# Performance work log

Measured on AMD Instinct MI355X. Metric: run time of the kernel, lower is better.

Reference implementation:

```python
import jax, jax.numpy as jnp
import numpy as np

D_MODEL, D_INNER, D_STATE, DT_RANK, D_CONV = 1024, 2048, 16, 64, 4
BATCH, SEQLEN = 2, 2048


def setup_inputs() -> dict:
    key = jax.random.key(0)
    ks = jax.random.split(key, 8)
    g = lambda k, shape, scale: jax.random.normal(k, shape, jnp.float32) * scale
    hidden_states = jax.random.normal(ks[0], (BATCH, SEQLEN, D_MODEL), jnp.float32)
    W_in = g(ks[1], (2 * D_INNER, D_MODEL), D_MODEL ** -0.5)
    conv_w = g(ks[2], (D_INNER, D_CONV), D_CONV ** -0.5)
    conv_b = jnp.zeros((D_INNER,), jnp.float32)
    W_x = g(ks[3], (DT_RANK + 2 * D_STATE, D_INNER), D_INNER ** -0.5)
    dt_init_std = DT_RANK ** -0.5  # dt_scale = 1.0
    W_dt = jax.random.uniform(ks[4], (D_INNER, DT_RANK), jnp.float32, -dt_init_std, dt_init_std)
    # faithful dt bias init: softplus^{-1}(dt) with dt ~ LogUniform(dt_min, dt_max)
    dt = jnp.exp(jax.random.uniform(ks[5], (D_INNER,), jnp.float32)
                 * (np.log(0.1) - np.log(0.001)) + np.log(0.001))
    dt = jnp.clip(dt, 1e-4)
    b_dt = dt + jnp.log(-jnp.expm1(-dt))
    A_log = jnp.log(jnp.broadcast_to(jnp.arange(1, D_STATE + 1, dtype=jnp.float32), (D_INNER, D_STATE)))
    D_param = jnp.ones((D_INNER,), jnp.float32)
    W_out = g(ks[6], (D_MODEL, D_INNER), D_INNER ** -0.5)
    return dict(hidden_states=hidden_states, W_in=W_in, conv_w=conv_w, conv_b=conv_b,
                W_x=W_x, W_dt=W_dt, b_dt=b_dt, A_log=A_log, D_param=D_param, W_out=W_out)


def reference(hidden_states, W_in, conv_w, conv_b, W_x, W_dt, b_dt, A_log, D_param, W_out):
    B_, L, _ = hidden_states.shape
    # in_proj (no bias) then split into x / gate z
    xz = jnp.einsum('bld,ed->ble', hidden_states, W_in)  # (B, L, 2*d_inner)
    x, z = jnp.split(xz, 2, axis=-1)
    # depthwise causal conv1d (padding = d_conv - 1, truncated to L)
    xp = jnp.pad(x, ((0, 0), (D_CONV - 1, 0), (0, 0)))
    xc = conv_b + sum(conv_w[:, k] * xp[:, k:k + L, :] for k in range(D_CONV))
    x = jax.nn.silu(xc)  # (B, L, d_inner)
    # input-dependent SSM params
    A = -jnp.exp(A_log)  # (d_inner, d_state)
    proj = jnp.einsum('bld,ed->ble', x, W_x)
    dt_lo, Bm, Cm = jnp.split(proj, [DT_RANK, DT_RANK + D_STATE], axis=-1)
    dt = jax.nn.softplus(jnp.einsum('blr,dr->bld', dt_lo, W_dt) + b_dt)  # (B, L, d_inner)
    # sequential selective scan: h = exp(dt*A)*h + dt*B*x ; y = C.h + D*x
    def step(h, inp):
        x_t, dt_t, B_t, C_t = inp  # (B,d), (B,d), (B,n), (B,n)
        dA = jnp.exp(dt_t[..., None] * A)                       # (B, d, n)
        h = dA * h + (dt_t * x_t)[..., None] * B_t[:, None, :]  # (B, d, n)
        y_t = jnp.einsum('bdn,bn->bd', h, C_t)
        return h, y_t

    h0 = jnp.zeros((B_, D_INNER, D_STATE), x.dtype)
    xs = (x.swapaxes(0, 1), dt.swapaxes(0, 1), Bm.swapaxes(0, 1), Cm.swapaxes(0, 1))
    _, ys = jax.lax.scan(step, h0, xs)
    y = ys.swapaxes(0, 1) + D_param * x
    y = y * jax.nn.silu(z)
    return jnp.einsum('bld,md->blm', y, W_out)
```

## Files before the change

kernel.cpp:

```cpp
#include <hip/hip_runtime.h>

typedef _Float16 f16;
typedef f16   f16x2 __attribute__((ext_vector_type(2)));
typedef f16   f16x4 __attribute__((ext_vector_type(4)));
typedef f16   f16x8 __attribute__((ext_vector_type(8)));
typedef float f32x2 __attribute__((ext_vector_type(2)));
typedef float f32x4 __attribute__((ext_vector_type(4)));

#define LOG2E 1.44269504088896f

__device__ __forceinline__ float fast_exp(float x) {
    return __builtin_amdgcn_exp2f(x * LOG2E);
}
__device__ __forceinline__ float silu_f(float x) {
    return x / (1.f + __builtin_amdgcn_exp2f(-LOG2E * x));
}
__device__ __forceinline__ float softplus_f(float x) {
    if (x > 16.f) return x;
    float e = __builtin_amdgcn_exp2f(x * LOG2E);
    return __builtin_amdgcn_logf(1.f + e) * 0.69314718056f;
}

#define DPP_ADD(x, ctrl) \
    ((x) + __int_as_float(__builtin_amdgcn_update_dpp(0, __float_as_int(x), (ctrl), 0xF, 0xF, true)))

__device__ __forceinline__ void gload_lds16(const void* g, void* l) {
    __builtin_amdgcn_global_load_lds((__attribute__((address_space(1))) void*)(g),
                                     (__attribute__((address_space(3))) void*)(l), 16, 0, 0);
}

__global__ __launch_bounds__(256) void cvt_all(const float* __restrict__ hidden, const float* __restrict__ W_in,
                                               const float* __restrict__ W_out, const float* __restrict__ W_dt,
                                               const float* __restrict__ W_x,
                                               f16* __restrict__ h16, f16* __restrict__ Win16,
                                               f16* __restrict__ Wout16, f16* __restrict__ Wdt16,
                                               f16* __restrict__ Wx16) {
    int i = blockIdx.x * 256 + threadIdx.x;
    const float* src;
    f16* dst;
    int idx;
    if (i < 1048576) { src = hidden; dst = h16; idx = i; }
    else if (i < 2097152) { src = W_in; dst = Win16; idx = i - 1048576; }
    else if (i < 2621440) { src = W_out; dst = Wout16; idx = i - 2097152; }
    else if (i < 2654208) { src = W_dt; dst = Wdt16; idx = i - 2621440; }
    else {
        int q = i - 2654208;
        int r = q >> 9;
        f32x4 v = {0.f, 0.f, 0.f, 0.f};
        if (r < 96) v = ((const f32x4*)W_x)[q];
        f16x4 o = {(f16)v[0], (f16)v[1], (f16)v[2], (f16)v[3]};
        ((f16x4*)Wx16)[q] = o;
        return;
    }
    f32x4 v = ((const f32x4*)src)[idx];
    f16x4 o = {(f16)v[0], (f16)v[1], (f16)v[2], (f16)v[3]};
    ((f16x4*)dst)[idx] = o;
}

__global__ void reduce_proj(const float* __restrict__ Pws, float* __restrict__ proj,
                            f16* __restrict__ dtlo) {
    int i = blockIdx.x * 256 + threadIdx.x;
    int m = i >> 5, c0 = (i & 31) * 4;
    f32x4 s = {0.f, 0.f, 0.f, 0.f};
#pragma unroll
    for (int z = 0; z < 8; z++)
        s += *(const f32x4*)(Pws + (size_t)z * 4096 * 128 + (size_t)m * 128 + c0);
    *(f32x4*)(proj + (size_t)m * 128 + c0) = s;
    if (c0 < 64) {
        f16x4 o = {(f16)s[0], (f16)s[1], (f16)s[2], (f16)s[3]};
        *(f16x4*)(dtlo + (size_t)m * 64 + c0) = o;
    }
}

__global__ __launch_bounds__(512) void gemm256(const f16* __restrict__ A, const f16* __restrict__ B,
                                               f16* __restrict__ C, int N, int K) {
    __shared__ f16 As[4][256 * 32];
    __shared__ f16 Bs[4][256 * 32];
    const int tid = threadIdx.x;
    const int w = tid >> 6, l = tid & 63;
    const int wr = w >> 2, wc = w & 3;
    const int lrow = l & 15, lkb = l >> 4;
    const int gpos = ((lkb ^ ((lrow >> 1) & 3)) * 8);
    const int bid = blockIdx.y * 16 + blockIdx.x;
    const int wg = (bid & 7) * 32 + (bid >> 3);
    const int mt = wg >> 4, nt = wg & 15;
    const int NT = K >> 5;

    f32x4 acc[8][4];
#pragma unroll
    for (int i = 0; i < 8; i++)
#pragma unroll
        for (int j = 0; j < 4; j++) acc[i][j] = (f32x4){0.f, 0.f, 0.f, 0.f};

    const int srow = w * 16 + (l >> 2);
    const int sgran = (l & 3) ^ ((l >> 3) & 3);
    const f16* Ag = A + (size_t)(mt * 256 + srow) * K + sgran * 8;
    const f16* Bg = B + (size_t)(nt * 256 + srow) * K + sgran * 8;

#define SCALL(s, kt, q)                                                        \
    do {                                                                       \
        if ((q) == 0) gload_lds16(Ag + (kt), &As[s][w * 512]);                 \
        if ((q) == 1) gload_lds16(Ag + (size_t)128 * K + (kt), &As[s][4096 + w * 512]); \
        if ((q) == 2) gload_lds16(Bg + (kt), &Bs[s][w * 512]);                 \
        if ((q) == 3) gload_lds16(Bg + (size_t)128 * K + (kt), &Bs[s][4096 + w * 512]); \
    } while (0)

#pragma unroll
    for (int q = 0; q < 4; ++q) SCALL(0, 0, q);
#pragma unroll
    for (int q = 0; q < 4; ++q) SCALL(1, 32, q);

    for (int t = 0; t < NT; ++t) {
        const f16* as = As[t & 3];
        const f16* bs = Bs[t & 3];
        const int pslot = (t + 2) & 3;
        const int pkt = ((t + 2 < NT) ? (t + 2) : (NT - 1)) * 32;

        asm volatile("s_waitcnt vmcnt(4)" ::: "memory");
        __builtin_amdgcn_sched_barrier(0);
        __builtin_amdgcn_s_barrier();
        __builtin_amdgcn_sched_barrier(0);

        f16x8 af[4], af2[4], bf[4];
#pragma unroll
        for (int i = 0; i < 4; i++)
            af[i] = *(const f16x8*)&as[(wr * 128 + i * 16 + lrow) * 32 + gpos];
#pragma unroll
        for (int j = 0; j < 4; j++)
            bf[j] = *(const f16x8*)&bs[(wc * 64 + j * 16 + lrow) * 32 + gpos];
        SCALL(pslot, pkt, 0);
        SCALL(pslot, pkt, 1);
        __builtin_amdgcn_s_barrier();
        __builtin_amdgcn_sched_barrier(0);
        __builtin_amdgcn_s_setprio(1);
#pragma unroll
        for (int i = 0; i < 4; i++)
#pragma unroll
            for (int j = 0; j < 4; j++)
                acc[i][j] = __builtin_amdgcn_mfma_f32_16x16x32_f16(af[i], bf[j], acc[i][j], 0, 0, 0);
        __builtin_amdgcn_s_setprio(0);

#pragma unroll
        for (int i = 0; i < 4; i++)
            af2[i] = *(const f16x8*)&as[(wr * 128 + 64 + i * 16 + lrow) * 32 + gpos];
        SCALL(pslot, pkt, 2);
        SCALL(pslot, pkt, 3);
        __builtin_amdgcn_s_barrier();
        __builtin_amdgcn_sched_barrier(0);
        __builtin_amdgcn_s_setprio(1);
#pragma unroll
        for (int i = 0; i < 4; i++)
#pragma unroll
            for (int j = 0; j < 4; j++)
                acc[i + 4][j] = __builtin_amdgcn_mfma_f32_16x16x32_f16(af2[i], bf[j], acc[i + 4][j], 0, 0, 0);
        __builtin_amdgcn_s_setprio(0);
    }
#undef SCALL

    const int orow = mt * 256 + wr * 128 + (l >> 4) * 4;
    const int ocol = nt * 256 + wc * 64 + lrow;
#pragma unroll
    for (int i = 0; i < 8; i++)
#pragma unroll
        for (int j = 0; j < 4; j++)
#pragma unroll
            for (int q = 0; q < 4; q++)
                C[(size_t)(orow + i * 16 + q) * N + ocol + j * 16] = (f16)acc[i][j][q];
}

__global__ __launch_bounds__(512) void gemm_out8(const f16* __restrict__ A, const f16* __restrict__ B,
                                                 float* __restrict__ C, int M, int N, int K) {
    __shared__ f16 As[4][128 * 64];
    __shared__ f16 Bs[4][128 * 64];
    const int tid = threadIdx.x;
    const int w = tid >> 6, l = tid & 63;
    const int wr = w >> 2, wc = w & 3;
    const int lrow = l & 15, lkb = l >> 4;
    const int swzr = lrow & 7;
    const int gx = gridDim.x;
    const int nwg = gx * gridDim.y;
    const int bid = blockIdx.y * gx + blockIdx.x;
    const int wg = (bid & 7) * (nwg >> 3) + (bid >> 3);
    const int nt = wg % gx, mt = wg / gx;
    const int NT = K >> 6;

    f32x4 acc[4][2];
#pragma unroll
    for (int i = 0; i < 4; i++)
#pragma unroll
        for (int j = 0; j < 2; j++) acc[i][j] = (f32x4){0.f, 0.f, 0.f, 0.f};

    const int srow = w * 8 + (l >> 3);
    const int sgran = (l & 7) ^ (l >> 3);
    const f16* Ag = A + (size_t)(mt * 128 + srow) * K + sgran * 8;
    const f16* Bg = B + (size_t)(nt * 128 + srow) * K + sgran * 8;

#define OCALL(s, kt, q)                                                                \
    do {                                                                               \
        if ((q) == 0) gload_lds16(Ag + (kt), &As[s][w * 512]);                         \
        if ((q) == 1) gload_lds16(Ag + (size_t)64 * K + (kt), &As[s][4096 + w * 512]); \
        if ((q) == 2) gload_lds16(Bg + (kt), &Bs[s][w * 512]);                         \
        if ((q) == 3) gload_lds16(Bg + (size_t)64 * K + (kt), &Bs[s][4096 + w * 512]); \
    } while (0)

#pragma unroll
    for (int q = 0; q < 4; ++q) OCALL(0, 0, q);
#pragma unroll
    for (int q = 0; q < 4; ++q) OCALL(1, 64, q);

    for (int t = 0; t < NT; ++t) {
        const f16* as = As[t & 3];
        const f16* bs = Bs[t & 3];
        const int pslot = (t + 2) & 3;
        const int pkt = ((t + 2 < NT) ? (t + 2) : (NT - 1)) * 64;

        asm volatile("s_waitcnt vmcnt(4)" ::: "memory");
        __builtin_amdgcn_sched_barrier(0);
        __builtin_amdgcn_s_barrier();
        __builtin_amdgcn_sched_barrier(0);

        f16x8 af[4], bf[2];
        {
            const int gp = ((lkb ^ swzr) * 8);
#pragma unroll
            for (int i = 0; i < 4; i++)
                af[i] = *(const f16x8*)&as[(wr * 64 + i * 16 + lrow) * 64 + gp];
#pragma unroll
            for (int j = 0; j < 2; j++)
                bf[j] = *(const f16x8*)&bs[(wc * 32 + j * 16 + lrow) * 64 + gp];
        }
        OCALL(pslot, pkt, 0);
        OCALL(pslot, pkt, 1);
        __builtin_amdgcn_s_barrier();
        __builtin_amdgcn_sched_barrier(0);
        __builtin_amdgcn_s_setprio(1);
#pragma unroll
        for (int i = 0; i < 4; i++)
#pragma unroll
            for (int j = 0; j < 2; j++)
                acc[i][j] = __builtin_amdgcn_mfma_f32_16x16x32_f16(af[i], bf[j], acc[i][j], 0, 0, 0);
        __builtin_amdgcn_s_setprio(0);

        {
            const int gp = (((4 + lkb) ^ swzr) * 8);
#pragma unroll
            for (int i = 0; i < 4; i++)
                af[i] = *(const f16x8*)&as[(wr * 64 + i * 16 + lrow) * 64 + gp];
#pragma unroll
            for (int j = 0; j < 2; j++)
                bf[j] = *(const f16x8*)&bs[(wc * 32 + j * 16 + lrow) * 64 + gp];
        }
        OCALL(pslot, pkt, 2);
        OCALL(pslot, pkt, 3);
        __builtin_amdgcn_s_barrier();
        __builtin_amdgcn_sched_barrier(0);
        __builtin_amdgcn_s_setprio(1);
#pragma unroll
        for (int i = 0; i < 4; i++)
#pragma unroll
            for (int j = 0; j < 2; j++)
                acc[i][j] = __builtin_amdgcn_mfma_f32_16x16x32_f16(af[i], bf[j], acc[i][j], 0, 0, 0);
        __builtin_amdgcn_s_setprio(0);
    }
#undef OCALL

    const int orow = mt * 128 + wr * 64 + (l >> 4) * 4;
    const int ocol = nt * 128 + wc * 32 + lrow;
#pragma unroll
    for (int i = 0; i < 4; i++)
#pragma unroll
        for (int j = 0; j < 2; j++)
#pragma unroll
            for (int q = 0; q < 4; q++)
                C[(size_t)(orow + i * 16 + q) * N + ocol + j * 16] = acc[i][j][q];
}

template <int EPI, typename OutT>
__global__ __launch_bounds__(256) void gemm_gl(const f16* __restrict__ A, const f16* __restrict__ B,
                                               OutT* __restrict__ C, const float* __restrict__ bias,
                                               int M, int N, int K, int kstep) {
    __shared__ f16 As[2][128 * 64];
    __shared__ f16 Bs[2][128 * 64];
    const int tid = threadIdx.x;
    const int w = tid >> 6, l = tid & 63;
    const int wm = (w >> 1) * 64, wn = (w & 1) * 64;
    const int lrow = l & 15, lkb = l >> 4;
    const int swzr = lrow & 7;
    const int gx = gridDim.x;
    const int nwg = gx * gridDim.y;
    const int bid = blockIdx.y * gx + blockIdx.x;
    const int wg = (bid & 7) * (nwg >> 3) + (bid >> 3);
    const int nt = wg % gx, mt = wg / gx;
    const int kbeg = blockIdx.z * kstep;
    const int NT = kstep >> 6;
    OutT* Cz = C + (size_t)blockIdx.z * M * N;

    f32x4 acc[4][4];
#pragma unroll
    for (int i = 0; i < 4; i++)
#pragma unroll
        for (int j = 0; j < 4; j++) acc[i][j] = (f32x4){0.f, 0.f, 0.f, 0.f};

    const int srow = w * 32 + (l >> 3);
    const int sgran = (l & 7) ^ (l >> 3);
    const f16* Ag = A + (size_t)(mt * 128 + srow) * K + sgran * 8 + kbeg;
    const f16* Bg = B + (size_t)(nt * 128 + srow) * K + sgran * 8 + kbeg;

#define STAGE128(s, kt)                                                         \
    do {                                                                        \
        _Pragma("unroll")                                                       \
        for (int i = 0; i < 4; ++i) {                                           \
            gload_lds16(Ag + (size_t)(i * 8) * K + (kt), &As[s][(w * 32 + i * 8) * 64]); \
            gload_lds16(Bg + (size_t)(i * 8) * K + (kt), &Bs[s][(w * 32 + i * 8) * 64]); \
        }                                                                       \
    } while (0)

    STAGE128(0, 0);
    __syncthreads();

    int cur = 0;
    for (int t = 0; t < NT; ++t) {
        if (t + 1 < NT) STAGE128(cur ^ 1, (t + 1) * 64);
#pragma unroll
        for (int kk = 0; kk < 64; kk += 32) {
            f16x8 af[4], bf[4];
            const int g = (kk >> 3) + lkb;
#pragma unroll
            for (int i = 0; i < 4; i++) {
                af[i] = *(const f16x8*)&As[cur][(wm + i * 16 + lrow) * 64 + ((g ^ swzr) * 8)];
                bf[i] = *(const f16x8*)&Bs[cur][(wn + i * 16 + lrow) * 64 + ((g ^ swzr) * 8)];
            }
#pragma unroll
            for (int i = 0; i < 4; i++)
#pragma unroll
                for (int j = 0; j < 4; j++)
                    acc[i][j] = __builtin_amdgcn_mfma_f32_16x16x32_f16(af[i], bf[j], acc[i][j], 0, 0, 0);
        }
        __syncthreads();
        cur ^= 1;
    }
#undef STAGE128

    const int orow = mt * 128 + wm + (l >> 4) * 4;
    const int ocol = nt * 128 + wn + lrow;
#pragma unroll
    for (int fm = 0; fm < 4; fm++)
#pragma unroll
        for (int fn = 0; fn < 4; fn++) {
            int c = ocol + fn * 16;
            float bv = (EPI == 1) ? bias[c] : 0.f;
#pragma unroll
            for (int i = 0; i < 4; i++) {
                float v = acc[fm][fn][i];
                if (EPI == 1) v = softplus_f(v + bv);
                Cz[(size_t)(orow + fm * 16 + i) * N + c] = (OutT)v;
            }
        }
}

__global__ __launch_bounds__(256) void conv_silu_k(const f16* __restrict__ xz, const float* __restrict__ cw,
                                                   const float* __restrict__ cb, f16* __restrict__ xc) {
    int idx = blockIdx.x * 256 + threadIdx.x;
    int m = idx >> 8;
    int d0 = (idx & 255) * 8;
    int l = m & 2047;
    float r[8];
    f32x4 cwv[8];
#pragma unroll
    for (int j = 0; j < 8; j++) {
        r[j] = cb[d0 + j];
        cwv[j] = *(const f32x4*)(cw + (size_t)(d0 + j) * 4);
    }
#pragma unroll
    for (int k = 0; k < 4; k++) {
        int ls = l - 3 + k;
        if (ls >= 0) {
            f16x8 xv = *(const f16x8*)(xz + (size_t)(m + k - 3) * 4096 + d0);
#pragma unroll
            for (int j = 0; j < 8; j++) r[j] += cwv[j][k] * (float)xv[j];
        }
    }
    f16x8 o;
#pragma unroll
    for (int j = 0; j < 8; j++) o[j] = (f16)silu_f(r[j]);
    *(f16x8*)(xc + (size_t)m * 2048 + d0) = o;
}

#define CT 32
#define NCHUNK 64
#define NSTATE 65536

__global__ __launch_bounds__(128) void scan_p1(const f16* __restrict__ dt16, const f16* __restrict__ xc,
                                               const float* __restrict__ proj, const float* __restrict__ A_log,
                                               f16* __restrict__ Pbuf, f16* __restrict__ Hend) {
    __shared__ float du_s[CT][32];
    __shared__ float bq_s[CT][20];
    const int tid = threadIdx.x;
    const int c = blockIdx.x, dg = blockIdx.y, b = blockIdx.z;
    const int d_base = dg << 5;
    const int g = tid >> 2, n = tid & 3;
    const int d = d_base + g;
    const float a0 = -fast_exp(A_log[d * 16 + n]) * LOG2E;
    const float a1 = -fast_exp(A_log[d * 16 + n + 4]) * LOG2E;
    const float a2 = -fast_exp(A_log[d * 16 + n + 8]) * LOG2E;
    const float a3 = -fast_exp(A_log[d * 16 + n + 12]) * LOG2E;
    const size_t mb = (size_t)b * 2048 + (size_t)c * CT;

    {
        const int trow = tid >> 2, seg = tid & 3, j0 = seg * 8;
        const size_t row = mb + trow;
        f16x8 dt8 = *(const f16x8*)(dt16 + row * 2048 + d_base + j0);
        f16x8 xc8 = *(const f16x8*)(xc + row * 2048 + d_base + j0);
#pragma unroll
        for (int k = 0; k < 8; ++k) {
            union { f16x2 h2; float f; } u;
            u.h2[0] = dt8[k];
            u.h2[1] = (f16)((float)dt8[k] * (float)xc8[k]);
            du_s[trow][j0 + k] = u.f;
        }
        f32x4 p0 = *(const f32x4*)(proj + row * 128 + 64 + seg * 4);
#pragma unroll
        for (int k = 0; k < 4; ++k) bq_s[trow][k * 4 + seg] = p0[k];
    }
    __syncthreads();

    float h0 = 0.f, h1 = 0.f, h2 = 0.f, h3 = 0.f, sdt = 0.f;
#pragma unroll 8
    for (int t = 0; t < CT; ++t) {
        union { float f; f16x2 h2; } u;
        u.f = du_s[t][g];
        float dtv = (float)u.h2[0], uv = (float)u.h2[1];
        f32x4 B4 = *(const f32x4*)&bq_s[t][n * 4];
        sdt += dtv;
        h0 = fmaf(__builtin_amdgcn_exp2f(dtv * a0), h0, uv * B4[0]);
        h1 = fmaf(__builtin_amdgcn_exp2f(dtv * a1), h1, uv * B4[1]);
        h2 = fmaf(__builtin_amdgcn_exp2f(dtv * a2), h2, uv * B4[2]);
        h3 = fmaf(__builtin_amdgcn_exp2f(dtv * a3), h3, uv * B4[3]);
    }
    const size_t base = (size_t)c * NSTATE + (size_t)(((b << 11) + d) * 16 + n * 4);
    f16x4 Pv = {(f16)__builtin_amdgcn_exp2f(a0 * sdt), (f16)__builtin_amdgcn_exp2f(a1 * sdt),
                (f16)__builtin_amdgcn_exp2f(a2 * sdt), (f16)__builtin_amdgcn_exp2f(a3 * sdt)};
    f16x4 Ev = {(f16)h0, (f16)h1, (f16)h2, (f16)h3};
    *(f16x4*)(Pbuf + base) = Pv;
    *(f16x4*)(Hend + base) = Ev;
}

__global__ __launch_bounds__(256) void scan_combine(const f16* __restrict__ Pbuf, const f16* __restrict__ Hend,
                                                    f16* __restrict__ Hinit) {
    int s2 = (blockIdx.x * 256 + threadIdx.x) * 2;
    float h0 = 0.f, h1 = 0.f;
#pragma unroll
    for (int c = 0; c < NCHUNK; c++) {
        size_t o = (size_t)c * NSTATE + s2;
        f16x2 P = *(const f16x2*)(Pbuf + o);
        f16x2 E = *(const f16x2*)(Hend + o);
        f16x2 Hi = {(f16)h0, (f16)h1};
        *(f16x2*)(Hinit + o) = Hi;
        h0 = fmaf((float)P[0], h0, (float)E[0]);
        h1 = fmaf((float)P[1], h1, (float)E[1]);
    }
}

__global__ __launch_bounds__(128) void scan_p2(const f16* __restrict__ dt16, const f16* __restrict__ xc,
                                               const f16* __restrict__ xz, const float* __restrict__ proj,
                                               const float* __restrict__ A_log, const float* __restrict__ Dp,
                                               const f16* __restrict__ Hinit, f16* __restrict__ y16) {
    __shared__ f32x2 dg_s[CT][32];
    __shared__ float bq_s[CT][20];
    __shared__ float cq_s[CT][20];
    const int tid = threadIdx.x;
    const int c = blockIdx.x, dg = blockIdx.y, b = blockIdx.z;
    const int d_base = dg << 5;
    const int g = tid >> 2, n = tid & 3;
    const int d = d_base + g;
    const float a0 = -fast_exp(A_log[d * 16 + n]) * LOG2E;
    const float a1 = -fast_exp(A_log[d * 16 + n + 4]) * LOG2E;
    const float a2 = -fast_exp(A_log[d * 16 + n + 8]) * LOG2E;
    const float a3 = -fast_exp(A_log[d * 16 + n + 12]) * LOG2E;
    const size_t mb = (size_t)b * 2048 + (size_t)c * CT;

    {
        const int trow = tid >> 2, seg = tid & 3, j0 = seg * 8;
        const size_t row = mb + trow;
        f16x8 dt8 = *(const f16x8*)(dt16 + row * 2048 + d_base + j0);
        f16x8 xc8 = *(const f16x8*)(xc + row * 2048 + d_base + j0);
        f16x8 xz8 = *(const f16x8*)(xz + row * 4096 + 2048 + d_base + j0);
        f32x4 dv0 = *(const f32x4*)(Dp + d_base + j0);
        f32x4 dv1 = *(const f32x4*)(Dp + d_base + j0 + 4);
#pragma unroll
        for (int k = 0; k < 8; ++k) {
            float dtv = (float)dt8[k], xv = (float)xc8[k];
            union { f16x2 h2; float f; } u;
            u.h2[0] = dt8[k];
            u.h2[1] = (f16)(dtv * xv);
            float sz = silu_f((float)xz8[k]);
            float Dv = (k < 4) ? dv0[k & 3] : dv1[k & 3];
            union { f16x2 h2; float f; } v;
            v.h2[0] = (f16)sz;
            v.h2[1] = (f16)(Dv * xv * sz);
            dg_s[trow][j0 + k] = (f32x2){u.f, v.f};
        }
        f32x4 pb0 = *(const f32x4*)(proj + row * 128 + 64 + seg * 4);
        f32x4 pc0 = *(const f32x4*)(proj + row * 128 + 80 + seg * 4);
#pragma unroll
        for (int k = 0; k < 4; ++k) {
            bq_s[trow][k * 4 + seg] = pb0[k];
            cq_s[trow][k * 4 + seg] = pc0[k];
        }
    }
    const size_t base = (size_t)c * NSTATE + (size_t)(((b << 11) + d) * 16 + n * 4);
    f16x4 H4 = *(const f16x4*)(Hinit + base);
    float h0 = (float)H4[0], h1 = (float)H4[1], h2 = (float)H4[2], h3 = (float)H4[3];
    __syncthreads();

#pragma unroll 8
    for (int t = 0; t < CT; ++t) {
        f32x2 dgv = dg_s[t][g];
        union { float f; f16x2 h2; } u;
        u.f = dgv[0];
        float dtv = (float)u.h2[0], uv = (float)u.h2[1];
        f32x4 B4 = *(const f32x4*)&bq_s[t][n * 4];
        f32x4 C4 = *(const f32x4*)&cq_s[t][n * 4];
        h0 = fmaf(__builtin_amdgcn_exp2f(dtv * a0), h0, uv * B4[0]);
        h1 = fmaf(__builtin_amdgcn_exp2f(dtv * a1), h1, uv * B4[1]);
        h2 = fmaf(__builtin_amdgcn_exp2f(dtv * a2), h2, uv * B4[2]);
        h3 = fmaf(__builtin_amdgcn_exp2f(dtv * a3), h3, uv * B4[3]);
        float yp = h0 * C4[0];
        yp = fmaf(h1, C4[1], yp);
        yp = fmaf(h2, C4[2], yp);
        yp = fmaf(h3, C4[3], yp);
        yp = DPP_ADD(yp, 0xB1);
        yp = DPP_ADD(yp, 0x4E);
        union { float f; f16x2 h2; } v;
        v.f = dgv[1];
        float yv = fmaf(yp, (float)v.h2[0], (float)v.h2[1]);
        if (n == 0) y16[(mb + t) * 2048 + d] = (f16)yv;
    }
}

extern "C" void kernel_launch(void* const* d_in, const int* in_sizes, int n_in,
                              void* d_out, int out_size, void* d_ws, size_t ws_size,
                              hipStream_t stream) {
    const float* hidden = (const float*)d_in[0];
    const float* W_in   = (const float*)d_in[1];
    const float* conv_w = (const float*)d_in[2];
    const float* conv_b = (const float*)d_in[3];
    const float* W_x    = (const float*)d_in[4];
    const float* W_dt   = (const float*)d_in[5];
    const float* b_dt   = (const float*)d_in[6];
    const float* A_log  = (const float*)d_in[7];
    const float* D_par  = (const float*)d_in[8];
    const float* W_out  = (const float*)d_in[9];
    float* out = (float*)d_out;

    char* ws = (char*)d_ws;
    size_t off = 0;
    auto alloc = [&](size_t bytes) { void* p = ws + off; off += (bytes + 255) & ~(size_t)255; return p; };
    f16* h16     = (f16*)alloc(4096ull * 1024 * 2);
    f16* Win16   = (f16*)alloc(4096ull * 1024 * 2);
    f16* Wx16    = (f16*)alloc(128ull * 2048 * 2);
    f16* Wdt16   = (f16*)alloc(2048ull * 64 * 2);
    f16* Wout16  = (f16*)alloc(1024ull * 2048 * 2);
    f16* xz16    = (f16*)alloc(4096ull * 4096 * 2);
    f16* xc16    = (f16*)alloc(4096ull * 2048 * 2);
    float* proj  = (float*)alloc(4096ull * 128 * 4);
    f16* dtlo16  = (f16*)alloc(4096ull * 64 * 2);
    f16* dt16    = (f16*)alloc(4096ull * 2048 * 2);
    f16* y16     = (f16*)alloc(4096ull * 2048 * 2);
    float* Pws   = (float*)y16;
    f16* Pbuf16  = (f16*)h16;
    f16* Hend16  = (f16*)y16;
    f16* Hinit16 = (f16*)Win16;
    (void)ws_size; (void)in_sizes; (void)n_in; (void)out_size;

    cvt_all<<<10624, 256, 0, stream>>>(hidden, W_in, W_out, W_dt, W_x,
                                       h16, Win16, Wout16, Wdt16, Wx16);

    gemm256<<<dim3(16, 16), 512, 0, stream>>>(h16, Win16, xz16, 4096, 1024);
    conv_silu_k<<<4096, 256, 0, stream>>>(xz16, conv_w, conv_b, xc16);
    gemm_gl<0, float><<<dim3(1, 32, 8), 256, 0, stream>>>(xc16, Wx16, Pws, nullptr, 4096, 128, 2048, 256);
    reduce_proj<<<512, 256, 0, stream>>>(Pws, proj, dtlo16);
    gemm_gl<1, f16><<<dim3(16, 32, 1), 256, 0, stream>>>(dtlo16, Wdt16, dt16, b_dt, 4096, 2048, 64, 64);
    scan_p1<<<dim3(NCHUNK, 64, 2), 128, 0, stream>>>(dt16, xc16, proj, A_log, Pbuf16, Hend16);
    scan_combine<<<128, 256, 0, stream>>>(Pbuf16, Hend16, Hinit16);
    scan_p2<<<dim3(NCHUNK, 64, 2), 128, 0, stream>>>(dt16, xc16, xz16, proj, A_log, D_par, Hinit16, y16);
    gemm_out8<<<dim3(8, 32), 512, 0, stream>>>(y16, Wout16, out, 4096, 1024, 2048);
}
```

Before: 190.3 us.

## Deepen GEMM prefetch to three stages, tile conv over time, and store split-K partials in fp16

Both LDS-pipelined GEMMs now prefetch three k-tiles ahead instead of two, using all four shared buffers, and wait on vmcnt(8) so more global loads stay in flight. The depthwise conv kernel now has each thread compute four consecutive timesteps from seven loaded rows, so overlapping input rows are reused instead of reloaded. The split-K partials for the x_proj GEMM are written and read as fp16 rather than fp32, which halves that workspace traffic but rounds the partial sums before reduction.

```diff
diff --git a/kernel.cpp b/kernel.cpp
--- a/kernel.cpp
+++ b/kernel.cpp
@@ -57,14 +57,16 @@
     ((f16x4*)dst)[idx] = o;
 }
 
-__global__ void reduce_proj(const float* __restrict__ Pws, float* __restrict__ proj,
+__global__ void reduce_proj(const f16* __restrict__ Pws, float* __restrict__ proj,
                             f16* __restrict__ dtlo) {
     int i = blockIdx.x * 256 + threadIdx.x;
     int m = i >> 5, c0 = (i & 31) * 4;
     f32x4 s = {0.f, 0.f, 0.f, 0.f};
 #pragma unroll
-    for (int z = 0; z < 8; z++)
-        s += *(const f32x4*)(Pws + (size_t)z * 4096 * 128 + (size_t)m * 128 + c0);
+    for (int z = 0; z < 8; z++) {
+        f16x4 p = *(const f16x4*)(Pws + (size_t)z * 4096 * 128 + (size_t)m * 128 + c0);
+        s += (f32x4){(float)p[0], (float)p[1], (float)p[2], (float)p[3]};
+    }
     *(f32x4*)(proj + (size_t)m * 128 + c0) = s;
     if (c0 < 64) {
         f16x4 o = {(f16)s[0], (f16)s[1], (f16)s[2], (f16)s[3]};
@@ -109,14 +111,16 @@
     for (int q = 0; q < 4; ++q) SCALL(0, 0, q);
 #pragma unroll
     for (int q = 0; q < 4; ++q) SCALL(1, 32, q);
+#pragma unroll
+    for (int q = 0; q < 4; ++q) SCALL(2, 64, q);
 
     for (int t = 0; t < NT; ++t) {
         const f16* as = As[t & 3];
         const f16* bs = Bs[t & 3];
-        const int pslot = (t + 2) & 3;
-        const int pkt = ((t + 2 < NT) ? (t + 2) : (NT - 1)) * 32;
-
-        asm volatile("s_waitcnt vmcnt(4)" ::: "memory");
+        const int pslot = (t + 3) & 3;
+        const int pkt = ((t + 3 < NT) ? (t + 3) : (NT - 1)) * 32;
+
+        asm volatile("s_waitcnt vmcnt(8)" ::: "memory");
         __builtin_amdgcn_sched_barrier(0);
         __builtin_amdgcn_s_barrier();
         __builtin_amdgcn_sched_barrier(0);
@@ -207,14 +211,16 @@
     for (int q = 0; q < 4; ++q) OCALL(0, 0, q);
 #pragma unroll
     for (int q = 0; q < 4; ++q) OCALL(1, 64, q);
+#pragma unroll
+    for (int q = 0; q < 4; ++q) OCALL(2, 128, q);
 
     for (int t = 0; t < NT; ++t) {
         const f16* as = As[t & 3];
         const f16* bs = Bs[t & 3];
-        const int pslot = (t + 2) & 3;
-        const int pkt = ((t + 2 < NT) ? (t + 2) : (NT - 1)) * 64;
-
-        asm volatile("s_waitcnt vmcnt(4)" ::: "memory");
+        const int pslot = (t + 3) & 3;
+        const int pkt = ((t + 3 < NT) ? (t + 3) : (NT - 1)) * 64;
+
+        asm volatile("s_waitcnt vmcnt(8)" ::: "memory");
         __builtin_amdgcn_sched_barrier(0);
         __builtin_amdgcn_s_barrier();
         __builtin_amdgcn_sched_barrier(0);
@@ -360,30 +366,39 @@
 
 __global__ __launch_bounds__(256) void conv_silu_k(const f16* __restrict__ xz, const float* __restrict__ cw,
                                                    const float* __restrict__ cb, f16* __restrict__ xc) {
-    int idx = blockIdx.x * 256 + threadIdx.x;
-    int m = idx >> 8;
-    int d0 = (idx & 255) * 8;
-    int l = m & 2047;
-    float r[8];
+    const int d0 = threadIdx.x * 8;
+    const int g = blockIdx.x;
+    const int b = g >> 9;
+    const int l0 = (g & 511) * 4;
+    const size_t mrow = (size_t)b * 2048 + l0;
     f32x4 cwv[8];
+    float r0[8];
 #pragma unroll
     for (int j = 0; j < 8; j++) {
-        r[j] = cb[d0 + j];
+        r0[j] = cb[d0 + j];
         cwv[j] = *(const f32x4*)(cw + (size_t)(d0 + j) * 4);
     }
-#pragma unroll
-    for (int k = 0; k < 4; k++) {
-        int ls = l - 3 + k;
-        if (ls >= 0) {
-            f16x8 xv = *(const f16x8*)(xz + (size_t)(m + k - 3) * 4096 + d0);
-#pragma unroll
-            for (int j = 0; j < 8; j++) r[j] += cwv[j][k] * (float)xv[j];
-        }
-    }
-    f16x8 o;
-#pragma unroll
-    for (int j = 0; j < 8; j++) o[j] = (f16)silu_f(r[j]);
-    *(f16x8*)(xc + (size_t)m * 2048 + d0) = o;
+    const f16x8 zero = {(f16)0.f, (f16)0.f, (f16)0.f, (f16)0.f, (f16)0.f, (f16)0.f, (f16)0.f, (f16)0.f};
+    f16x8 xv[7];
+#pragma unroll
+    for (int i = 0; i < 7; ++i) {
+        int ls = l0 - 3 + i;
+        xv[i] = (ls >= 0) ? *(const f16x8*)(xz + (mrow - 3 + i) * 4096 + d0) : zero;
+    }
+#pragma unroll
+    for (int tt = 0; tt < 4; ++tt) {
+        float r[8];
+#pragma unroll
+        for (int j = 0; j < 8; j++) r[j] = r0[j];
+#pragma unroll
+        for (int k = 0; k < 4; k++)
+#pragma unroll
+            for (int j = 0; j < 8; j++) r[j] += cwv[j][k] * (float)xv[tt + k][j];
+        f16x8 o;
+#pragma unroll
+        for (int j = 0; j < 8; j++) o[j] = (f16)silu_f(r[j]);
+        *(f16x8*)(xc + (mrow + tt) * 2048 + d0) = o;
+    }
 }
 
 #define CT 32
@@ -567,7 +582,7 @@
     f16* dtlo16  = (f16*)alloc(4096ull * 64 * 2);
     f16* dt16    = (f16*)alloc(4096ull * 2048 * 2);
     f16* y16     = (f16*)alloc(4096ull * 2048 * 2);
-    float* Pws   = (float*)y16;
+    f16* Pws     = (f16*)y16;
     f16* Pbuf16  = (f16*)h16;
     f16* Hend16  = (f16*)y16;
     f16* Hinit16 = (f16*)Win16;
@@ -577,8 +592,8 @@
                                        h16, Win16, Wout16, Wdt16, Wx16);
 
     gemm256<<<dim3(16, 16), 512, 0, stream>>>(h16, Win16, xz16, 4096, 1024);
-    conv_silu_k<<<4096, 256, 0, stream>>>(xz16, conv_w, conv_b, xc16);
-    gemm_gl<0, float><<<dim3(1, 32, 8), 256, 0, stream>>>(xc16, Wx16, Pws, nullptr, 4096, 128, 2048, 256);
+    conv_silu_k<<<1024, 256, 0, stream>>>(xz16, conv_w, conv_b, xc16);
+    gemm_gl<0, f16><<<dim3(1, 32, 8), 256, 0, stream>>>(xc16, Wx16, Pws, nullptr, 4096, 128, 2048, 256);
     reduce_proj<<<512, 256, 0, stream>>>(Pws, proj, dtlo16);
     gemm_gl<1, f16><<<dim3(16, 32, 1), 256, 0, stream>>>(dtlo16, Wdt16, dt16, b_dt, 4096, 2048, 64, 64);
     scan_p1<<<dim3(NCHUNK, 64, 2), 128, 0, stream>>>(dt16, xc16, proj, A_log, Pbuf16, Hend16);
```

Result: faster. 176.5 us (-7.2%).
